# Kernel tuning notes

Measured on AMD Instinct MI355X. Metric: run time of the kernel, lower is better.

## Reference

```python
import jax, jax.numpy as jnp
import numpy as np

B, N = 16, 2048
EMBED_DIM = 72
K = 40                      # k_neighbors
NUM_STAGES = 4
ALPHA, BETA = 1000.0, 100.0
STAGE_DIMS = [(144, 72), (288, 144), (576, 32), (1152, 576)]  # (out_dim, hidden); stage 2 is the 32-d adapter
EPS = 1e-5


def _bn(x, g, b, axes):
    # training-mode batch norm (biased variance), channel axis = 1
    m = jnp.mean(x, axes, keepdims=True)
    v = jnp.var(x, axes, keepdims=True)
    sh = (1, -1) + (1,) * (x.ndim - 2)
    return (x - m) / jnp.sqrt(v + EPS) * g.reshape(sh) + b.reshape(sh)


def setup_inputs() -> dict:
    key = jax.random.key(0)
    ks = iter(jax.random.split(key, 40))
    d = {}
    d["xyz"] = jax.random.normal(next(ks), (B, N, 3), jnp.float32)
    d["x"] = jax.random.normal(next(ks), (B, 3, N), jnp.float32)
    d["embed_w"] = jax.random.normal(next(ks), (EMBED_DIM, 3), jnp.float32) * 0.1
    d["embed_g"] = jnp.ones((EMBED_DIM,), jnp.float32)
    d["embed_b"] = jnp.zeros((EMBED_DIM,), jnp.float32)
    for i, (o, h) in enumerate(STAGE_DIMS):
        d[f"s{i}_w1"] = jax.random.normal(next(ks), (h, o), jnp.float32) * 0.05
        d[f"s{i}_b1"] = jnp.zeros((h,), jnp.float32)
        d[f"s{i}_g1"] = jnp.ones((h,), jnp.float32)
        d[f"s{i}_bb1"] = jnp.zeros((h,), jnp.float32)
        d[f"s{i}_w2"] = jax.random.normal(next(ks), (o, h), jnp.float32) * 0.05
        d[f"s{i}_b2"] = jnp.zeros((o,), jnp.float32)
        d[f"s{i}_g2"] = jnp.ones((o,), jnp.float32)
        d[f"s{i}_bb2"] = jnp.zeros((o,), jnp.float32)
    return d


def _forward(xyz, x, embed_w, embed_g, embed_b, stage_params):
    # raw point embed: 1x1 Conv1d (no bias) + BN + ReLU -> [B, 72, N]
    feats = jax.nn.relu(_bn(jnp.einsum('bcn,oc->bon', x, embed_w), embed_g, embed_b, (0, 2)))
    for i in range(NUM_STAGES):
        out_dim = STAGE_DIMS[i][0]
        n_cur = xyz.shape[1]
        g = n_cur // 2
        pts = feats.transpose(0, 2, 1)                                  # [B, n_cur, C]
        # torch code overwrites FPS with random indices -> faithful random sampling
        fps_idx = jax.random.randint(jax.random.key(1000 + i), (B, g), 0, n_cur)
        lc_xyz = jnp.take_along_axis(xyz, fps_idx[:, :, None], axis=1)  # [B, g, 3]
        lc_x = jnp.take_along_axis(pts, fps_idx[:, :, None], axis=1)    # [B, g, C]
        # squared pairwise distances [B, g, n_cur]
        d2 = (-2.0 * jnp.einsum('bgc,bnc->bgn', lc_xyz, xyz)
              + jnp.sum(lc_xyz ** 2, -1)[:, :, None]
              + jnp.sum(xyz ** 2, -1)[:, None, :])
        _, knn_idx = jax.lax.top_k(-d2, K)                              # [B, g, K] smallest dists
        knn_xyz = jax.vmap(lambda p, ix: p[ix])(xyz, knn_idx)           # [B, g, K, 3]
        knn_x = jax.vmap(lambda p, ix: p[ix])(pts, knn_idx)             # [B, g, K, C]
        # LGA, type='mn40': center + global-std normalize (torch.std is unbiased)
        diff = knn_xyz - lc_xyz[:, :, None, :]
        knn_xyz_n = diff / (jnp.std(diff, ddof=1) + 1e-5)
        # concat neighbor feats with center feats -> channels 2C == out_dim
        kx = jnp.concatenate([knn_x, jnp.broadcast_to(lc_x[:, :, None, :], knn_x.shape)], -1)
        kx = kx.transpose(0, 3, 1, 2)                                   # [B, out_dim, g, K]
        kz = knn_xyz_n.transpose(0, 3, 1, 2)                            # [B, 3, g, K]
        # PosE_Geo
        f = out_dim // 6
        dim_embed = ALPHA ** (jnp.arange(f, dtype=kx.dtype) / f)
        div = BETA * kz[..., None] / dim_embed                          # [B, 3, g, K, f]
        pe = jnp.concatenate([jnp.sin(div), jnp.cos(div)], -1)          # [B, 3, g, K, 2f]
        pe = pe.transpose(0, 1, 4, 2, 3).reshape(B, out_dim, g, K)
        w = kx + pe
        # Linear2Layer: relu(bn(conv(relu(bn(conv(w))))) + w)
        w1, b1, g1, bb1, w2, b2, g2, bb2 = stage_params[i]
        h = jax.nn.relu(_bn(jnp.einsum('bcgk,oc->bogk', w, w1) + b1[None, :, None, None], g1, bb1, (0, 2, 3)))
        h = _bn(jnp.einsum('bcgk,oc->bogk', h, w2) + b2[None, :, None, None], g2, bb2, (0, 2, 3))
        w = jax.nn.relu(h + w)
        feats = jnp.max(w, -1)                                          # pooling over K -> [B, out_dim, g]
        xyz = lc_xyz
    return xyz, feats


def reference(xyz, x, embed_w, embed_g, embed_b,
              s0_w1, s0_b1, s0_g1, s0_bb1, s0_w2, s0_b2, s0_g2, s0_bb2,
              s1_w1, s1_b1, s1_g1, s1_bb1, s1_w2, s1_b2, s1_g2, s1_bb2,
              s2_w1, s2_b1, s2_g1, s2_bb1, s2_w2, s2_b2, s2_g2, s2_bb2,
              s3_w1, s3_b1, s3_g1, s3_bb1, s3_w2, s3_b2, s3_g2, s3_bb2):
    sp = [(s0_w1, s0_b1, s0_g1, s0_bb1, s0_w2, s0_b2, s0_g2, s0_bb2),
          (s1_w1, s1_b1, s1_g1, s1_bb1, s1_w2, s1_b2, s1_g2, s1_bb2),
          (s2_w1, s2_b1, s2_g1, s2_bb1, s2_w2, s2_b2, s2_g2, s2_bb2),
          (s3_w1, s3_b1, s3_g1, s3_bb1, s3_w2, s3_b2, s3_g2, s3_bb2)]
    return _forward(xyz, x, embed_w, embed_g, embed_b, sp)
```

## Files before the change

kernel.cpp:

```cpp
#include <hip/hip_runtime.h>
#include <stdint.h>
#include <math.h>

#define KNB 40
static constexpr int NB = 16;

using short8 = __attribute__((ext_vector_type(8))) short;
using f32x4  = __attribute__((ext_vector_type(4))) float;

static constexpr size_t OFF_W4  = 0;
static constexpr size_t OFF_Hb  = 47185920;
static constexpr size_t OFF_FA  = 141557760;
static constexpr size_t OFF_FB  = 150994944;
static constexpr size_t OFF_FT  = 160432128;
static constexpr size_t OFF_XA  = 169869312;
static constexpr size_t OFF_XB  = 170065920;
static constexpr size_t OFF_FPS = 170262528;
static constexpr size_t OFF_KNN = 170328064;
static constexpr size_t OFF_W1H = 172949504;
static constexpr size_t OFF_W1L = 174276608;
static constexpr size_t OFF_W2H = 175603712;
static constexpr size_t OFF_W2L = 176930816;
static constexpr size_t OFF_SUM = 178257920;
static constexpr size_t OFF_SQ  = 178294784;
static constexpr size_t OFF_SC1 = 178331648;
static constexpr size_t OFF_SH1 = 178336256;
static constexpr size_t OFF_SC2 = 178340864;
static constexpr size_t OFF_SH2 = 178345472;
static constexpr size_t OFF_DST = 178350080;
static constexpr size_t OFF_INV = 178350096;

__device__ static inline float bf2f(uint16_t h){ return __uint_as_float(((uint32_t)h) << 16); }
__device__ static inline uint16_t f2bf(float f){
  uint32_t u = __float_as_uint(f);
  uint32_t r = u + 0x7fffu + ((u >> 16) & 1u);
  return (uint16_t)(r >> 16);
}

__device__ static inline void gload_lds16(const void* g, void* l){
  __builtin_amdgcn_global_load_lds((const __attribute__((address_space(1))) uint32_t*)g,
                                   (__attribute__((address_space(3))) uint32_t*)l, 16, 0, 0);
}

__host__ __device__ static inline uint32_t rotl32(uint32_t v, int d){ return (v<<d)|(v>>(32-d)); }
#define TF_RND(r) { x0 += x1; x1 = rotl32(x1,(r)); x1 ^= x0; }
__host__ __device__ static inline void tf2x32(uint32_t k0, uint32_t k1, uint32_t& x0, uint32_t& x1){
  uint32_t ks2 = k0 ^ k1 ^ 0x1BD11BDAu;
  x0 += k0; x1 += k1;
  TF_RND(13) TF_RND(15) TF_RND(26) TF_RND(6)   x0 += k1;  x1 += ks2 + 1u;
  TF_RND(17) TF_RND(29) TF_RND(16) TF_RND(24)  x0 += ks2; x1 += k0 + 2u;
  TF_RND(13) TF_RND(15) TF_RND(26) TF_RND(6)   x0 += k0;  x1 += k1 + 3u;
  TF_RND(17) TF_RND(29) TF_RND(16) TF_RND(24)  x0 += k1;  x1 += ks2 + 4u;
  TF_RND(13) TF_RND(15) TF_RND(26) TF_RND(6)   x0 += ks2; x1 += k0 + 5u;
}

__device__ static inline float freq_of(int t, int f){
  return exp2f(-((float)t / (float)f) * 9.965784284662087f);
}

__global__ __launch_bounds__(256) void k_embed(const float* __restrict__ x,
                                               const float* __restrict__ w,
                                               float* __restrict__ out){
  __shared__ float sw[216];
  int t = threadIdx.x;
  if (t < 216) sw[t] = w[t];
  __syncthreads();
  int gid = blockIdx.x*256 + t;
  int n = gid & 2047, b = gid >> 11;
  float x0 = x[((size_t)b*3+0)*2048 + n];
  float x1 = x[((size_t)b*3+1)*2048 + n];
  float x2 = x[((size_t)b*3+2)*2048 + n];
  #pragma unroll 4
  for (int o = 0; o < 72; ++o){
    float v = sw[o*3]*x0 + sw[o*3+1]*x1 + sw[o*3+2]*x2;
    out[((size_t)b*72 + o)*2048 + n] = v;
  }
}

__global__ __launch_bounds__(256) void k_chan_stats_f32(const float* __restrict__ in, int C, int M,
                                                        float* __restrict__ SUMf, float* __restrict__ SQf){
  int c = blockIdx.x, b = blockIdx.y;
  const float* p = in + ((size_t)b*C + c)*M;
  float s = 0.f, s2 = 0.f;
  for (int m = threadIdx.x; m < M; m += 256){ float v = p[m]; s += v; s2 += v*v; }
  __shared__ float sa[256], sb[256];
  int t = threadIdx.x;
  sa[t] = s; sb[t] = s2; __syncthreads();
  for (int o = 128; o > 0; o >>= 1){
    if (t < o){ sa[t] += sa[t+o]; sb[t] += sb[t+o]; }
    __syncthreads();
  }
  if (t == 0){ atomicAdd(&SUMf[c], sa[0]); atomicAdd(&SQf[c], sb[0]); }
}

__global__ void k_bn_finalize8(const float* __restrict__ SUMf, const float* __restrict__ SQf,
                               int C, double Mn, const float* __restrict__ gamma,
                               const float* __restrict__ beta, float* __restrict__ scale,
                               float* __restrict__ shift){
  int c = blockIdx.x*blockDim.x + threadIdx.x;
  if (c >= C) return;
  float s = 0.f, q = 0.f;
  #pragma unroll
  for (int k = 0; k < 8; ++k){ s += SUMf[k*1152 + c]; q += SQf[k*1152 + c]; }
  double mean = (double)s / Mn;
  double var = (double)q / Mn - mean*mean;
  if (var < 0.0) var = 0.0;
  float sc = gamma[c] / sqrtf((float)var + 1e-5f);
  scale[c] = sc;
  shift[c] = beta[c] - (float)mean * sc;
}

__global__ __launch_bounds__(256) void k_bn_apply(float* __restrict__ buf,
                                                  const float* __restrict__ scale,
                                                  const float* __restrict__ shift,
                                                  int C, int M, long long total){
  long long idx = (long long)blockIdx.x*256 + threadIdx.x;
  if (idx >= total) return;
  int c = (int)((idx / M) % C);
  float v = buf[idx]*scale[c] + shift[c];
  buf[idx] = fmaxf(v, 0.f);
}

__global__ __launch_bounds__(256) void k_transpose(const float* __restrict__ in,
                                                   float* __restrict__ out, int C, int ncur){
  long long idx = (long long)blockIdx.x*256 + threadIdx.x;
  long long total = (long long)NB*ncur*C;
  if (idx >= total) return;
  int c = (int)(idx % C);
  int n = (int)((idx / C) % ncur);
  int b = (int)(idx / ((long long)C*ncur));
  out[idx] = in[((size_t)b*C + c)*ncur + n];
}

__global__ __launch_bounds__(256) void k_wconv_tiled(const float* __restrict__ w,
                                                     uint16_t* __restrict__ hi,
                                                     int Cout, int Cin){
  int i = blockIdx.x*256 + threadIdx.x;
  if (i >= Cout*Cin) return;
  int row = i / Cin, k = i - row*Cin;
  size_t o = (((size_t)(row>>4)*(Cin>>3) + (k>>3))*16 + (row&15))*8 + (k&7);
  hi[o] = f2bf(w[i]);
}

__global__ __launch_bounds__(256) void k_fps(const float* __restrict__ xyz, float* __restrict__ lc,
                                             int* __restrict__ fps, int ncur, int g,
                                             uint32_t ka, uint32_t kb){
  int m = blockIdx.x*256 + threadIdx.x;
  int total = NB * g;
  if (m >= total) return;
  uint32_t x0 = 0u, x1 = (uint32_t)m;
  tf2x32(ka, kb, x0, x1);
  uint32_t v = x0 ^ x1;
  int idx = (int)(v & (uint32_t)(ncur - 1));
  fps[m] = idx;
  int b = m / g;
  const float* s = xyz + ((size_t)b*ncur + idx)*3;
  float* d = lc + (size_t)m*3;
  d[0] = s[0]; d[1] = s[1]; d[2] = s[2];
}

__global__ __launch_bounds__(256) void k_final_xyz(const float* __restrict__ xyz0,
                                                   float* __restrict__ out,
                                                   uint32_t ka0, uint32_t kb0,
                                                   uint32_t ka1, uint32_t kb1,
                                                   uint32_t ka2, uint32_t kb2,
                                                   uint32_t ka3, uint32_t kb3){
  int m = blockIdx.x*256 + threadIdx.x;
  if (m >= 2048) return;
  int b = m >> 7;
  uint32_t x0, x1;
  x0 = 0u; x1 = (uint32_t)m;        tf2x32(ka3, kb3, x0, x1);
  uint32_t i3 = (x0 ^ x1) & 255u;
  x0 = 0u; x1 = (uint32_t)b*256u + i3;  tf2x32(ka2, kb2, x0, x1);
  uint32_t i2 = (x0 ^ x1) & 511u;
  x0 = 0u; x1 = (uint32_t)b*512u + i2;  tf2x32(ka1, kb1, x0, x1);
  uint32_t i1 = (x0 ^ x1) & 1023u;
  x0 = 0u; x1 = (uint32_t)b*1024u + i1; tf2x32(ka0, kb0, x0, x1);
  uint32_t i0 = (x0 ^ x1) & 2047u;
  const float* s = xyz0 + ((size_t)b*2048 + i0)*3;
  out[(size_t)m*3+0] = s[0];
  out[(size_t)m*3+1] = s[1];
  out[(size_t)m*3+2] = s[2];
}

template<int CNT>
__global__ __launch_bounds__(64) void k_knn(const float* __restrict__ xyz,
                                            const float* __restrict__ lc,
                                            int* __restrict__ knn, int ncur, int g){
  int row = blockIdx.x;
  int b = row / g;
  int lane = threadIdx.x;
  float lx = lc[row*3+0], ly = lc[row*3+1], lz = lc[row*3+2];
  float ln = lx*lx + ly*ly + lz*lz;
  const float* xb = xyz + (size_t)b*ncur*3;
  unsigned long long pk[CNT];
  #pragma unroll
  for (int t = 0; t < CNT; ++t){
    int n = lane + 64*t;
    float px = xb[n*3+0], py = xb[n*3+1], pz = xb[n*3+2];
    float dot = lx*px + ly*py + lz*pz;
    float pn = px*px + py*py + pz*pz;
    float d2 = -2.0f*dot + ln + pn;
    unsigned u = __float_as_uint(d2);
    if (u == 0x80000000u) u = 0u;
    unsigned su = (u & 0x80000000u) ? ~u : (u | 0x80000000u);
    pk[t] = ((unsigned long long)su << 32) | (unsigned)n;
  }
  for (int it = 0; it < KNB; ++it){
    unsigned long long m = ~0ull;
    #pragma unroll
    for (int t = 0; t < CNT; ++t) m = (pk[t] < m) ? pk[t] : m;
    #pragma unroll
    for (int s = 1; s < 64; s <<= 1){
      unsigned long long o = __shfl_xor(m, s, 64);
      m = (o < m) ? o : m;
    }
    if (lane == 0) knn[(size_t)row*KNB + it] = (int)(unsigned)(m & 0xffffffffu);
    #pragma unroll
    for (int t = 0; t < CNT; ++t) if (pk[t] == m) pk[t] = ~0ull;
  }
}

__global__ __launch_bounds__(256) void k_diff_stats(const float* __restrict__ xyz,
                                                    const float* __restrict__ lc,
                                                    const int* __restrict__ knn,
                                                    int ncur, int g, double* __restrict__ out){
  long long gid = (long long)blockIdx.x*256 + threadIdx.x;
  long long total = (long long)NB*g*KNB;
  double s = 0.0, s2 = 0.0;
  if (gid < total){
    long long jj = gid / KNB;
    int nn = knn[gid];
    const float* p = xyz + ((size_t)(jj/g)*ncur + nn)*3;
    const float* c = lc + (size_t)jj*3;
    #pragma unroll
    for (int a = 0; a < 3; ++a){ float df = p[a] - c[a]; double d = (double)df; s += d; s2 += d*d; }
  }
  __shared__ double sa[256], sb[256];
  int t = threadIdx.x;
  sa[t] = s; sb[t] = s2; __syncthreads();
  for (int o = 128; o > 0; o >>= 1){
    if (t < o){ sa[t] += sa[t+o]; sb[t] += sb[t+o]; }
    __syncthreads();
  }
  if (t == 0){ atomicAdd(&out[0], sa[0]); atomicAdd(&out[1], sb[0]); }
}

__global__ void k_scalar_fin(const double* __restrict__ dst, double Mn, float* __restrict__ inv_std){
  double s = dst[0], s2 = dst[1];
  double mean = s / Mn;
  double var = (s2 - s*mean) / (Mn - 1.0);
  if (var < 0.0) var = 0.0;
  float stdv = sqrtf((float)var);
  *inv_std = 1.0f / (stdv + 1e-5f);
}

__global__ __launch_bounds__(256) void k_build_w8(const float* __restrict__ featsT,
                                                  const float* __restrict__ xyz,
                                                  const float* __restrict__ lc,
                                                  const int* __restrict__ fps,
                                                  const int* __restrict__ knn,
                                                  const float* __restrict__ inv_std,
                                                  uint16_t* __restrict__ W4,
                                                  int C, int g, int ncur, int f, int b0){
  long long idx = (long long)blockIdx.x*256 + threadIdx.x;
  int C2 = 6*f;
  int C8 = C2 >> 3;
  int M = g*KNB;
  int M16 = M >> 4;
  long long total = 4LL*M16*C8*16;
  if (idx >= total) return;
  int n_in = (int)(idx & 15);
  long long r2 = idx >> 4;
  int c8 = (int)(r2 % C8);
  long long r3 = r2 / C8;
  int n16 = (int)(r3 % M16);
  int bl = (int)(r3 / M16);
  int b = b0 + bl;
  int n = n16*16 + n_in;
  int j = n / KNB;
  int k = n - j*KNB;
  int nn = knn[((size_t)(b*g+j))*KNB + k];
  float is = *inv_std;
  int ch0 = c8*8;
  int axis = ch0 / (2*f);
  float diff = xyz[((size_t)b*ncur + nn)*3 + axis] - lc[((size_t)(b*g+j))*3 + axis];
  float base = 100.0f * (diff * is);
  bool isCtr = (ch0 >= C);
  int src = isCtr ? fps[b*g+j] : nn;
  const float* fsrc = featsT + ((size_t)b*ncur + src)*C + (isCtr ? (ch0 - C) : ch0);
  int r0_ = ch0 % (2*f);
  bool sinb = (r0_ < f);
  int t0 = sinb ? r0_ : (r0_ - f);
  short8 sv;
  #pragma unroll
  for (int e = 0; e < 8; ++e){
    float fr = freq_of(t0 + e, f);
    float arg = base * fr;
    float pe = sinb ? __sinf(arg) : __cosf(arg);
    sv[e] = (short)f2bf(fsrc[e] + pe);
  }
  size_t woff = (((size_t)bl*M16 + n16)*(size_t)C8 + c8)*128 + (size_t)n_in*8;
  *(short8*)(W4 + woff) = sv;
}

__global__ __launch_bounds__(256) void k_bn1_relu(uint16_t* __restrict__ H,
                                                  const float* __restrict__ sc, const float* __restrict__ sh,
                                                  int K8, long long total){
  long long idx = (long long)blockIdx.x*256 + threadIdx.x;
  if (idx >= total) return;
  int c = (int)((idx >> 7) % K8)*8 + (int)(idx & 7);
  float v = bf2f(H[idx]) * sc[c] + sh[c];
  H[idx] = f2bf(fmaxf(v, 0.f));
}

template<int MODE, int NSUB>
__global__ __launch_bounds__(256) void k_mfma_tile(
    const uint16_t* __restrict__ Ahi,
    const uint16_t* __restrict__ Bmat,
    const float* __restrict__ bias,
    uint16_t* __restrict__ Hout,
    float* __restrict__ SUMf, float* __restrict__ SQf,
    const float* __restrict__ sc2, const float* __restrict__ sh2,
    const float* __restrict__ featsT,
    const float* __restrict__ xyz, const float* __restrict__ lc,
    const int* __restrict__ fps, const int* __restrict__ knn,
    const float* __restrict__ inv_std, float* __restrict__ fout,
    int Cout, int Cin, int M, int b0, int C, int g, int ncur, int f, int RY)
{
  __shared__ unsigned lmax[1152];
  __shared__ uint16_t c2t[64*130];
  __shared__ float dls[64][3];
  __shared__ int nnls[64], ctrls[64];
  __shared__ uint16_t Bst[2][2048];
  int bz = blockIdx.z; int b = b0 + bz;
  int lin = blockIdx.x;
  int GXW = (int)gridDim.x / (8*RY);
  int xcd = lin & 7;
  int slot = lin >> 3;
  int sdiv = slot / RY;
  int bx = xcd*GXW + sdiv;
  int ry = slot - sdiv*RY;
  int r0 = ry * 128;
  int tid = threadIdx.x;
  int w = tid >> 6, l = tid & 63;
  int lr = l & 15, kg = l >> 4;
  int rw = r0 + w*32;
  const short8 zf = (short8){0,0,0,0,0,0,0,0};

  if (MODE == 2){
    for (int e = tid; e < 1152; e += 256) lmax[e] = 0u;
    __syncthreads();
  }
  float sacc[2][4] = {{0.f,0.f,0.f,0.f},{0.f,0.f,0.f,0.f}};
  float qacc[2][4] = {{0.f,0.f,0.f,0.f},{0.f,0.f,0.f,0.f}};
  float is = (MODE == 2) ? *inv_std : 0.f;

  int K8 = Cin >> 3;
  int T = (Cin + 31) >> 5;
  int rw16 = rw >> 4;
  const size_t aoff0 = ((size_t)(rw16+0)*K8)*128 + (size_t)lr*8;
  const size_t aoff1 = ((size_t)(rw16+1)*K8)*128 + (size_t)lr*8;
  bool rv0 = (rw + lr) < Cout, rv1 = (rw + 16 + lr) < Cout;
  const uint16_t* Bbat = Bmat + (size_t)bz*(M>>4)*(size_t)K8*128;

  for (int sub = 0; sub < NSUB; ++sub){
    int n0 = bx*(64*NSUB) + sub*64;
    int nb0 = n0 >> 4;
    const uint16_t* srcW = Bbat + ((size_t)(nb0 + w)*K8)*128 + (size_t)l*8;
    f32x4 acc[2][4];
    #pragma unroll
    for (int i = 0; i < 2; ++i)
      #pragma unroll
      for (int j = 0; j < 4; ++j) acc[i][j] = (f32x4){0.f,0.f,0.f,0.f};

    gload_lds16(srcW, &Bst[0][w*512]);
    short8 ahc[2];
    {
      int kb = kg;
      bool kv = kb < K8;
      ahc[0] = (kv && rv0) ? *(const short8*)(Ahi + aoff0 + (size_t)kb*128) : zf;
      ahc[1] = (kv && rv1) ? *(const short8*)(Ahi + aoff1 + (size_t)kb*128) : zf;
    }
    __syncthreads();

    for (int t = 0; t < T; ++t){
      int buf = t & 1;
      bool more = (t + 1) < T;
      if (more) gload_lds16(srcW + (size_t)(t+1)*512, &Bst[buf^1][w*512]);
      short8 ahn[2];
      int kbn = (t+1)*4 + kg;
      bool kvn = kbn < K8;
      if (more){
        ahn[0] = (kvn && rv0) ? *(const short8*)(Ahi + aoff0 + (size_t)kbn*128) : zf;
        ahn[1] = (kvn && rv1) ? *(const short8*)(Ahi + aoff1 + (size_t)kbn*128) : zf;
      }
      short8 bvc[4];
      int kb = t*4 + kg;
      bool kv = kb < K8;
      #pragma unroll
      for (int nf = 0; nf < 4; ++nf){
        short8 bv = *(const short8*)(&Bst[buf][nf*512 + l*8]);
        bvc[nf] = kv ? bv : zf;
      }
      #pragma unroll
      for (int nf = 0; nf < 4; ++nf){
        acc[0][nf] = __builtin_amdgcn_mfma_f32_16x16x32_bf16(ahc[0], bvc[nf], acc[0][nf], 0, 0, 0);
        acc[1][nf] = __builtin_amdgcn_mfma_f32_16x16x32_bf16(ahc[1], bvc[nf], acc[1][nf], 0, 0, 0);
      }
      if (more){ ahc[0] = ahn[0]; ahc[1] = ahn[1]; }
      __syncthreads();
    }

    if (MODE == 0 || MODE == 1){
      int K8h = Cout >> 3;
      #pragma unroll
      for (int rf = 0; rf < 2; ++rf){
        int chbase = rw + rf*16 + kg*4;
        bool cv = chbase < Cout;
        float bz4[4];
        #pragma unroll
        for (int r = 0; r < 4; ++r) bz4[r] = cv ? bias[chbase + r] : 0.f;
        #pragma unroll
        for (int nf = 0; nf < 4; ++nf){
          float v0 = acc[rf][nf][0] + bz4[0];
          float v1 = acc[rf][nf][1] + bz4[1];
          float v2 = acc[rf][nf][2] + bz4[2];
          float v3 = acc[rf][nf][3] + bz4[3];
          if (MODE == 0 && cv){
            ushort4 st = make_ushort4(f2bf(v0), f2bf(v1), f2bf(v2), f2bf(v3));
            size_t hoff = ((((size_t)b*(M>>4) + nb0 + nf)*K8h + (chbase>>3))*16 + lr)*8 + (chbase&7);
            *(ushort4*)(Hout + hoff) = st;
          }
          sacc[rf][0]+=v0; qacc[rf][0]+=v0*v0;
          sacc[rf][1]+=v1; qacc[rf][1]+=v1*v1;
          sacc[rf][2]+=v2; qacc[rf][2]+=v2*v2;
          sacc[rf][3]+=v3; qacc[rf][3]+=v3*v3;
        }
      }
    } else {
      if (tid < 64){
        int col = tid;
        int n = n0 + col;
        int j = n / KNB;
        int kq = n - j*KNB;
        int nn = knn[((size_t)(b*g+j))*KNB + kq];
        #pragma unroll
        for (int a = 0; a < 3; ++a){
          float diff = xyz[((size_t)b*ncur + nn)*3 + a] - lc[((size_t)(b*g+j))*3 + a];
          dls[col][a] = 100.0f * (diff * is);
        }
        nnls[col] = nn;
        ctrls[col] = fps[b*g+j];
      }
      #pragma unroll
      for (int rf = 0; rf < 2; ++rf){
        int chl = w*32 + rf*16 + kg*4;
        int ch = r0 + chl;
        if (ch < Cout){
          float b0_ = bias[ch+0], b1_ = bias[ch+1], b2_ = bias[ch+2], b3_ = bias[ch+3];
          float m0 = sc2[ch+0], m1 = sc2[ch+1], m2_ = sc2[ch+2], m3 = sc2[ch+3];
          float a0 = sh2[ch+0], a1 = sh2[ch+1], a2_ = sh2[ch+2], a3 = sh2[ch+3];
          #pragma unroll
          for (int nf = 0; nf < 4; ++nf){
            int col = nf*16 + lr;
            float v0 = m0*(acc[rf][nf][0] + b0_) + a0;
            float v1 = m1*(acc[rf][nf][1] + b1_) + a1;
            float v2 = m2_*(acc[rf][nf][2] + b2_) + a2_;
            float v3 = m3*(acc[rf][nf][3] + b3_) + a3;
            uint32_t p0 = (uint32_t)f2bf(v0) | ((uint32_t)f2bf(v1) << 16);
            uint32_t p1 = (uint32_t)f2bf(v2) | ((uint32_t)f2bf(v3) << 16);
            *(uint32_t*)&c2t[col*130 + chl]     = p0;
            *(uint32_t*)&c2t[col*130 + chl + 2] = p1;
          }
        }
      }
      __syncthreads();
      {
        int chl = tid & 127, half = tid >> 7;
        int ch = r0 + chl;
        if (ch < Cout){
          int axis = ch / (2*f);
          int r = ch % (2*f);
          int t = (r < f) ? r : r - f;
          float fr = freq_of(t, f);
          bool isCtr = (ch >= C);
          int chF = isCtr ? (ch - C) : ch;
          int curj = -1; float curmax = 0.f;
          #pragma unroll 4
          for (int cc = 0; cc < 32; ++cc){
            int col = half*32 + cc;
            int n = n0 + col;
            int j = n / KNB;
            float arg = dls[col][axis] * fr;
            float pe = (r < f) ? __sinf(arg) : __cosf(arg);
            int src = isCtr ? ctrls[col] : nnls[col];
            float kx = featsT[((size_t)b*ncur + src)*C + chF];
            float v = fmaxf(bf2f(c2t[col*130 + chl]) + kx + pe, 0.f);
            if (j != curj){
              if (curj >= 0) atomicMax(&lmax[chl*9 + (curj - bx*8)], __float_as_uint(curmax));
              curj = j; curmax = v;
            } else {
              curmax = fmaxf(curmax, v);
            }
          }
          atomicMax(&lmax[chl*9 + (curj - bx*8)], __float_as_uint(curmax));
        }
      }
      __syncthreads();
    }
  }

  if (MODE == 0 || MODE == 1){
    int sl = (bx & 7)*1152;
    #pragma unroll
    for (int rf = 0; rf < 2; ++rf){
      int chbase = rw + rf*16 + kg*4;
      bool cv = chbase < Cout;
      #pragma unroll
      for (int r = 0; r < 4; ++r){
        float ss = sacc[rf][r], qq = qacc[rf][r];
        ss += __shfl_xor(ss, 1, 64); qq += __shfl_xor(qq, 1, 64);
        ss += __shfl_xor(ss, 2, 64); qq += __shfl_xor(qq, 2, 64);
        ss += __shfl_xor(ss, 4, 64); qq += __shfl_xor(qq, 4, 64);
        ss += __shfl_xor(ss, 8, 64); qq += __shfl_xor(qq, 8, 64);
        if (cv && lr == 0){
          atomicAdd(&SUMf[sl + chbase + r], ss);
          atomicAdd(&SQf[sl + chbase + r], qq);
        }
      }
    }
  } else {
    for (int e = tid; e < 1024; e += 256){
      int chloc = e >> 3, jloc = e & 7;
      int ch = r0 + chloc;
      if (ch < Cout)
        fout[((size_t)b*Cout + ch)*g + bx*8 + jloc] = __uint_as_float(lmax[chloc*9 + jloc]);
    }
  }
}

extern "C" void kernel_launch(void* const* d_in, const int* in_sizes, int n_in,
                              void* d_out, int out_size, void* d_ws, size_t ws_size,
                              hipStream_t stream){
  (void)in_sizes; (void)n_in; (void)out_size; (void)ws_size;
  const float* xyz0 = (const float*)d_in[0];
  const float* xin  = (const float*)d_in[1];
  const float* ew   = (const float*)d_in[2];
  const float* eg   = (const float*)d_in[3];
  const float* ebb  = (const float*)d_in[4];

  char* ws = (char*)d_ws;
  uint16_t* W4  = (uint16_t*)(ws + OFF_W4);
  uint16_t* Hb  = (uint16_t*)(ws + OFF_Hb);
  float* FA  = (float*)(ws + OFF_FA);
  float* FB  = (float*)(ws + OFF_FB);
  float* FT  = (float*)(ws + OFF_FT);
  float* XA  = (float*)(ws + OFF_XA);
  float* XB  = (float*)(ws + OFF_XB);
  int*   FPS = (int*)(ws + OFF_FPS);
  int*   KNN = (int*)(ws + OFF_KNN);
  uint16_t* W1H = (uint16_t*)(ws + OFF_W1H);
  uint16_t* W2H = (uint16_t*)(ws + OFF_W2H);
  float* SUMf = (float*)(ws + OFF_SUM);
  float* SQf  = (float*)(ws + OFF_SQ);
  float* SC1 = (float*)(ws + OFF_SC1);
  float* SH1 = (float*)(ws + OFF_SH1);
  float* SC2 = (float*)(ws + OFF_SC2);
  float* SH2 = (float*)(ws + OFF_SH2);
  double* DST = (double*)(ws + OFF_DST);
  float* INV  = (float*)(ws + OFF_INV);
  float* out = (float*)d_out;

  uint32_t KA[4], KB[4];
  for (int i = 0; i < 4; ++i){
    uint32_t a = 0u, c = 1u; tf2x32(0u, (uint32_t)(1000+i), a, c);
    KA[i] = a; KB[i] = c;
  }

  k_embed<<<128, 256, 0, stream>>>(xin, ew, FA);
  hipMemsetAsync(SUMf, 0, 2*36864, stream);
  k_chan_stats_f32<<<dim3(72, NB), 256, 0, stream>>>(FA, 72, 2048, SUMf, SQf);
  k_bn_finalize8<<<1, 256, 0, stream>>>(SUMf, SQf, 72, 32768.0, eg, ebb, SC1, SH1);
  {
    long long tot = 16LL*72*2048;
    k_bn_apply<<<(int)((tot+255)/256), 256, 0, stream>>>(FA, SC1, SH1, 72, 2048, tot);
  }

  const int Cins[4] = {72,144,288,576};
  const int hids[4] = {72,144,32,576};
  const float* xcur = xyz0;
  float* fcur = FA;

  for (int i = 0; i < 4; ++i){
    int ncur = 2048 >> i, g = ncur >> 1;
    int C = Cins[i], C2 = 2*C, hid = hids[i], f = C2/6, M = g*KNB;
    float* lc = (i & 1) ? XB : XA;
    float* fout = (i < 3) ? ((i & 1) ? FA : FB) : (out + 6144);
    const float* w1  = (const float*)d_in[5+i*8+0];
    const float* b1  = (const float*)d_in[5+i*8+1];
    const float* g1  = (const float*)d_in[5+i*8+2];
    const float* bb1 = (const float*)d_in[5+i*8+3];
    const float* w2  = (const float*)d_in[5+i*8+4];
    const float* b2  = (const float*)d_in[5+i*8+5];
    const float* g2  = (const float*)d_in[5+i*8+6];
    const float* bb2 = (const float*)d_in[5+i*8+7];

    {
      long long tot = (long long)NB*ncur*C;
      k_transpose<<<(int)((tot+255)/256), 256, 0, stream>>>(fcur, FT, C, ncur);
    }
    k_wconv_tiled<<<(hid*C2+255)/256, 256, 0, stream>>>(w1, W1H, hid, C2);
    k_wconv_tiled<<<(C2*hid+255)/256, 256, 0, stream>>>(w2, W2H, C2, hid);

    int tot_fps = NB*g;
    k_fps<<<(tot_fps+255)/256, 256, 0, stream>>>(xcur, lc, FPS, ncur, g, KA[i], KB[i]);

    if (ncur == 2048)      k_knn<32><<<NB*g, 64, 0, stream>>>(xcur, lc, KNN, ncur, g);
    else if (ncur == 1024) k_knn<16><<<NB*g, 64, 0, stream>>>(xcur, lc, KNN, ncur, g);
    else if (ncur == 512)  k_knn< 8><<<NB*g, 64, 0, stream>>>(xcur, lc, KNN, ncur, g);
    else                   k_knn< 4><<<NB*g, 64, 0, stream>>>(xcur, lc, KNN, ncur, g);

    hipMemsetAsync(DST, 0, 16, stream);
    int totk = NB*g*KNB;
    k_diff_stats<<<(totk+255)/256, 256, 0, stream>>>(xcur, lc, KNN, ncur, g, DST);
    k_scalar_fin<<<1, 1, 0, stream>>>(DST, (double)totk * 3.0, INV);

    int GX64 = M/64;
    int GX320 = M/320;
    hipMemsetAsync(SUMf, 0, 2*36864, stream);
    long long totw8 = 4LL*(M>>4)*(C2>>3)*16;
    int ry1 = (hid + 127)/128;
    for (int c = 0; c < 4; ++c){
      k_build_w8<<<(int)((totw8+255)/256), 256, 0, stream>>>(FT, xcur, lc, FPS, KNN, INV, W4, C, g, ncur, f, c*4);
      k_mfma_tile<0,1><<<dim3(GX64*ry1, 1, 4), 256, 0, stream>>>(
          W1H, W4, b1, Hb, SUMf, SQf,
          nullptr, nullptr, nullptr, nullptr, nullptr, nullptr, nullptr, nullptr, nullptr,
          hid, C2, M, c*4, C, g, ncur, f, ry1);
    }
    k_bn_finalize8<<<(hid+255)/256, 256, 0, stream>>>(SUMf, SQf, hid, (double)NB*M, g1, bb1, SC1, SH1);

    {
      long long tot = (long long)NB*M*hid;
      k_bn1_relu<<<(int)((tot+255)/256), 256, 0, stream>>>(Hb, SC1, SH1, hid>>3, tot);
    }

    hipMemsetAsync(SUMf, 0, 2*36864, stream);
    int ry2 = (C2 + 127)/128;
    k_mfma_tile<1,1><<<dim3(GX64*ry2, 1, NB), 256, 0, stream>>>(
        W2H, Hb, b2, nullptr, SUMf, SQf,
        nullptr, nullptr, nullptr, nullptr, nullptr, nullptr, nullptr, nullptr, nullptr,
        C2, hid, M, 0, C, g, ncur, f, ry2);
    k_bn_finalize8<<<(C2+255)/256, 256, 0, stream>>>(SUMf, SQf, C2, (double)NB*M, g2, bb2, SC2, SH2);

    k_mfma_tile<2,5><<<dim3(GX320*ry2, 1, NB), 256, 0, stream>>>(
        W2H, Hb, b2, nullptr, nullptr, nullptr,
        SC2, SH2, FT, xcur, lc, FPS, KNN, INV, fout,
        C2, hid, M, 0, C, g, ncur, f, ry2);

    xcur = lc; fcur = fout;
  }

  k_final_xyz<<<8, 256, 0, stream>>>(xyz0, out, KA[0], KB[0], KA[1], KB[1],
                                     KA[2], KB[2], KA[3], KB[3]);
}
```

Baseline: 3.730 ms.

## Deepen MFMA B prefetch to 4-step groups, tile transpose, vectorize BN1 ReLU

The MFMA GEMM kernel now stages four K-steps of the B operand into LDS per group, double-buffered, instead of one step at a time. This means fewer barriers per K-loop, and the LDS is shared with the epilogue scratch through a union. The A operand is now loaded directly inside each step rather than prefetched one step ahead, which may expose global-load latency. The feature transpose becomes an LDS-tiled 64x64 transpose so both reads and writes are coalesced, and the BN1+ReLU pass handles four bf16 values per thread with 8-byte accesses.

```diff
diff --git a/kernel.cpp b/kernel.cpp
--- a/kernel.cpp
+++ b/kernel.cpp
@@ -18,9 +18,7 @@
 static constexpr size_t OFF_FPS = 170262528;
 static constexpr size_t OFF_KNN = 170328064;
 static constexpr size_t OFF_W1H = 172949504;
-static constexpr size_t OFF_W1L = 174276608;
 static constexpr size_t OFF_W2H = 175603712;
-static constexpr size_t OFF_W2L = 176930816;
 static constexpr size_t OFF_SUM = 178257920;
 static constexpr size_t OFF_SQ  = 178294784;
 static constexpr size_t OFF_SC1 = 178331648;
@@ -123,13 +121,23 @@
 
 __global__ __launch_bounds__(256) void k_transpose(const float* __restrict__ in,
                                                    float* __restrict__ out, int C, int ncur){
-  long long idx = (long long)blockIdx.x*256 + threadIdx.x;
-  long long total = (long long)NB*ncur*C;
-  if (idx >= total) return;
-  int c = (int)(idx % C);
-  int n = (int)((idx / C) % ncur);
-  int b = (int)(idx / ((long long)C*ncur));
-  out[idx] = in[((size_t)b*C + c)*ncur + n];
+  __shared__ float tile[64][65];
+  int b = blockIdx.z;
+  int n0 = blockIdx.x * 64;
+  int c0 = blockIdx.y * 64;
+  int tx = threadIdx.x & 63, ty = threadIdx.x >> 6;
+  #pragma unroll
+  for (int r = 0; r < 64; r += 4){
+    int c = c0 + r + ty;
+    if (c < C) tile[r + ty][tx] = in[((size_t)b*C + c)*ncur + n0 + tx];
+  }
+  __syncthreads();
+  #pragma unroll
+  for (int r = 0; r < 64; r += 4){
+    int n = n0 + r + ty;
+    int c = c0 + tx;
+    if (c < C) out[((size_t)b*ncur + n)*C + c] = tile[tx][r + ty];
+  }
 }
 
 __global__ __launch_bounds__(256) void k_wconv_tiled(const float* __restrict__ w,
@@ -304,14 +312,24 @@
   *(short8*)(W4 + woff) = sv;
 }
 
-__global__ __launch_bounds__(256) void k_bn1_relu(uint16_t* __restrict__ H,
-                                                  const float* __restrict__ sc, const float* __restrict__ sh,
-                                                  int K8, long long total){
-  long long idx = (long long)blockIdx.x*256 + threadIdx.x;
-  if (idx >= total) return;
-  int c = (int)((idx >> 7) % K8)*8 + (int)(idx & 7);
-  float v = bf2f(H[idx]) * sc[c] + sh[c];
-  H[idx] = f2bf(fmaxf(v, 0.f));
+__global__ __launch_bounds__(256) void k_bn1_relu4(uint16_t* __restrict__ H,
+                                                   const float* __restrict__ sc, const float* __restrict__ sh,
+                                                   int K8, long long total4){
+  long long i = (long long)blockIdx.x*256 + threadIdx.x;
+  if (i >= total4) return;
+  long long e0 = i << 2;
+  int cb = (int)((e0 >> 7) % K8)*8 + (int)(e0 & 7);
+  uint2 v = *(uint2*)(H + e0);
+  uint16_t h0 = (uint16_t)(v.x & 0xffff), h1 = (uint16_t)(v.x >> 16);
+  uint16_t h2 = (uint16_t)(v.y & 0xffff), h3 = (uint16_t)(v.y >> 16);
+  float r0 = fmaxf(bf2f(h0)*sc[cb+0] + sh[cb+0], 0.f);
+  float r1 = fmaxf(bf2f(h1)*sc[cb+1] + sh[cb+1], 0.f);
+  float r2 = fmaxf(bf2f(h2)*sc[cb+2] + sh[cb+2], 0.f);
+  float r3 = fmaxf(bf2f(h3)*sc[cb+3] + sh[cb+3], 0.f);
+  uint2 o;
+  o.x = (uint32_t)f2bf(r0) | ((uint32_t)f2bf(r1) << 16);
+  o.y = (uint32_t)f2bf(r2) | ((uint32_t)f2bf(r3) << 16);
+  *(uint2*)(H + e0) = o;
 }
 
 template<int MODE, int NSUB>
@@ -329,10 +347,15 @@
     int Cout, int Cin, int M, int b0, int C, int g, int ncur, int f, int RY)
 {
   __shared__ unsigned lmax[1152];
-  __shared__ uint16_t c2t[64*130];
-  __shared__ float dls[64][3];
-  __shared__ int nnls[64], ctrls[64];
-  __shared__ uint16_t Bst[2][2048];
+  __shared__ union ShU {
+    uint16_t bst[2][4][2048];
+    struct {
+      uint16_t c2t[64*130];
+      float dls[64][3];
+      int nnls[64];
+      int ctrls[64];
+    } epi;
+  } sh;
   int bz = blockIdx.z; int b = b0 + bz;
   int lin = blockIdx.x;
   int GXW = (int)gridDim.x / (8*RY);
@@ -358,6 +381,7 @@
 
   int K8 = Cin >> 3;
   int T = (Cin + 31) >> 5;
+  int NG = (T + 3) >> 2;
   int rw16 = rw >> 4;
   const size_t aoff0 = ((size_t)(rw16+0)*K8)*128 + (size_t)lr*8;
   const size_t aoff1 = ((size_t)(rw16+1)*K8)*128 + (size_t)lr*8;
@@ -374,41 +398,43 @@
       #pragma unroll
       for (int j = 0; j < 4; ++j) acc[i][j] = (f32x4){0.f,0.f,0.f,0.f};
 
-    gload_lds16(srcW, &Bst[0][w*512]);
-    short8 ahc[2];
-    {
-      int kb = kg;
-      bool kv = kb < K8;
-      ahc[0] = (kv && rv0) ? *(const short8*)(Ahi + aoff0 + (size_t)kb*128) : zf;
-      ahc[1] = (kv && rv1) ? *(const short8*)(Ahi + aoff1 + (size_t)kb*128) : zf;
+    #pragma unroll
+    for (int s = 0; s < 4; ++s){
+      int t = (s < T) ? s : (T - 1);
+      gload_lds16(srcW + (size_t)t*512, &sh.bst[0][s][w*512]);
     }
     __syncthreads();
 
-    for (int t = 0; t < T; ++t){
-      int buf = t & 1;
-      bool more = (t + 1) < T;
-      if (more) gload_lds16(srcW + (size_t)(t+1)*512, &Bst[buf^1][w*512]);
-      short8 ahn[2];
-      int kbn = (t+1)*4 + kg;
-      bool kvn = kbn < K8;
-      if (more){
-        ahn[0] = (kvn && rv0) ? *(const short8*)(Ahi + aoff0 + (size_t)kbn*128) : zf;
-        ahn[1] = (kvn && rv1) ? *(const short8*)(Ahi + aoff1 + (size_t)kbn*128) : zf;
-      }
-      short8 bvc[4];
-      int kb = t*4 + kg;
-      bool kv = kb < K8;
-      #pragma unroll
-      for (int nf = 0; nf < 4; ++nf){
-        short8 bv = *(const short8*)(&Bst[buf][nf*512 + l*8]);
-        bvc[nf] = kv ? bv : zf;
+    for (int grp = 0; grp < NG; ++grp){
+      int buf = grp & 1;
+      if (grp + 1 < NG){
+        #pragma unroll
+        for (int s = 0; s < 4; ++s){
+          int tt = (grp+1)*4 + s; if (tt > T-1) tt = T-1;
+          gload_lds16(srcW + (size_t)tt*512, &sh.bst[buf^1][s][w*512]);
+        }
       }
       #pragma unroll
-      for (int nf = 0; nf < 4; ++nf){
-        acc[0][nf] = __builtin_amdgcn_mfma_f32_16x16x32_bf16(ahc[0], bvc[nf], acc[0][nf], 0, 0, 0);
-        acc[1][nf] = __builtin_amdgcn_mfma_f32_16x16x32_bf16(ahc[1], bvc[nf], acc[1][nf], 0, 0, 0);
+      for (int s = 0; s < 4; ++s){
+        int t = grp*4 + s;
+        if (t < T){
+          int kb = t*4 + kg;
+          bool kv = kb < K8;
+          short8 ah0 = (kv && rv0) ? *(const short8*)(Ahi + aoff0 + (size_t)kb*128) : zf;
+          short8 ah1 = (kv && rv1) ? *(const short8*)(Ahi + aoff1 + (size_t)kb*128) : zf;
+          short8 bv[4];
+          #pragma unroll
+          for (int nf = 0; nf < 4; ++nf){
+            short8 bvv = *(const short8*)(&sh.bst[buf][s][nf*512 + l*8]);
+            bv[nf] = kv ? bvv : zf;
+          }
+          #pragma unroll
+          for (int nf = 0; nf < 4; ++nf){
+            acc[0][nf] = __builtin_amdgcn_mfma_f32_16x16x32_bf16(ah0, bv[nf], acc[0][nf], 0, 0, 0);
+            acc[1][nf] = __builtin_amdgcn_mfma_f32_16x16x32_bf16(ah1, bv[nf], acc[1][nf], 0, 0, 0);
+          }
+        }
       }
-      if (more){ ahc[0] = ahn[0]; ahc[1] = ahn[1]; }
       __syncthreads();
     }
 
@@ -448,10 +474,10 @@
         #pragma unroll
         for (int a = 0; a < 3; ++a){
           float diff = xyz[((size_t)b*ncur + nn)*3 + a] - lc[((size_t)(b*g+j))*3 + a];
-          dls[col][a] = 100.0f * (diff * is);
+          sh.epi.dls[col][a] = 100.0f * (diff * is);
         }
-        nnls[col] = nn;
-        ctrls[col] = fps[b*g+j];
+        sh.epi.nnls[col] = nn;
+        sh.epi.ctrls[col] = fps[b*g+j];
       }
       #pragma unroll
       for (int rf = 0; rf < 2; ++rf){
@@ -470,8 +496,8 @@
             float v3 = m3*(acc[rf][nf][3] + b3_) + a3;
             uint32_t p0 = (uint32_t)f2bf(v0) | ((uint32_t)f2bf(v1) << 16);
             uint32_t p1 = (uint32_t)f2bf(v2) | ((uint32_t)f2bf(v3) << 16);
-            *(uint32_t*)&c2t[col*130 + chl]     = p0;
-            *(uint32_t*)&c2t[col*130 + chl + 2] = p1;
+            *(uint32_t*)&sh.epi.c2t[col*130 + chl]     = p0;
+            *(uint32_t*)&sh.epi.c2t[col*130 + chl + 2] = p1;
           }
         }
       }
@@ -492,11 +518,11 @@
             int col = half*32 + cc;
             int n = n0 + col;
             int j = n / KNB;
-            float arg = dls[col][axis] * fr;
+            float arg = sh.epi.dls[col][axis] * fr;
             float pe = (r < f) ? __sinf(arg) : __cosf(arg);
-            int src = isCtr ? ctrls[col] : nnls[col];
+            int src = isCtr ? sh.epi.ctrls[col] : sh.epi.nnls[col];
             float kx = featsT[((size_t)b*ncur + src)*C + chF];
-            float v = fmaxf(bf2f(c2t[col*130 + chl]) + kx + pe, 0.f);
+            float v = fmaxf(bf2f(sh.epi.c2t[col*130 + chl]) + kx + pe, 0.f);
             if (j != curj){
               if (curj >= 0) atomicMax(&lmax[chl*9 + (curj - bx*8)], __float_as_uint(curmax));
               curj = j; curmax = v;
@@ -606,10 +632,7 @@
     const float* g2  = (const float*)d_in[5+i*8+6];
     const float* bb2 = (const float*)d_in[5+i*8+7];
 
-    {
-      long long tot = (long long)NB*ncur*C;
-      k_transpose<<<(int)((tot+255)/256), 256, 0, stream>>>(fcur, FT, C, ncur);
-    }
+    k_transpose<<<dim3(ncur/64, (C+63)/64, NB), 256, 0, stream>>>(fcur, FT, C, ncur);
     k_wconv_tiled<<<(hid*C2+255)/256, 256, 0, stream>>>(w1, W1H, hid, C2);
     k_wconv_tiled<<<(C2*hid+255)/256, 256, 0, stream>>>(w2, W2H, C2, hid);
 
@@ -641,8 +664,8 @@
     k_bn_finalize8<<<(hid+255)/256, 256, 0, stream>>>(SUMf, SQf, hid, (double)NB*M, g1, bb1, SC1, SH1);
 
     {
-      long long tot = (long long)NB*M*hid;
-      k_bn1_relu<<<(int)((tot+255)/256), 256, 0, stream>>>(Hb, SC1, SH1, hid>>3, tot);
+      long long tot4 = ((long long)NB*M*hid) >> 2;
+      k_bn1_relu4<<<(int)((tot4+255)/256), 256, 0, stream>>>(Hb, SC1, SH1, hid>>3, tot4);
     }
 
     hipMemsetAsync(SUMf, 0, 2*36864, stream);
```

Measured after the change: 3.789 ms. Within noise of the previous version (+1.6%).
